# Kernel tuning notes

Measured on AMD Instinct MI355X. Metric: run time of the kernel, lower is better.

The kernel has to match this reference:

```python
import jax, jax.numpy as jnp
import numpy as np

B, N, D = 64, 128, 32
P = N * (N - 1)          # ordered pairs
H1, H2, HF = 32, 32, 16  # layer_widths=(32,32), final_widths=(16,)
EPS = 1e-5
SLOPE = 0.01             # LeakyReLU default


def _leaky(x):
    return jnp.where(x >= 0, x, SLOPE * x)


def setup_inputs() -> dict:
    key = jax.random.key(0)
    ks = jax.random.split(key, 16)
    # all ordered pairs (i, j), i != j, grouped by source i
    src = np.repeat(np.arange(N), N - 1)
    tgt = np.array([j for i in range(N) for j in range(N) if j != i])
    s = 0.1
    return {
        "inputs": jax.random.normal(ks[0], (B, N, D), jnp.float32),
        "src": jnp.asarray(src, jnp.int32),
        "tgt": jnp.asarray(tgt, jnp.int32),
        # edge MLP: Linear(2D,32) -> BN1d(P) -> LeakyReLU -> Linear(32,32) -> LeakyReLU -> Linear(32, 1+D)
        "W1": jax.random.normal(ks[1], (2 * D, H1), jnp.float32) * s,
        "b1": jnp.zeros((H1,), jnp.float32),
        "g1": jnp.ones((P,), jnp.float32),
        "be1": jnp.zeros((P,), jnp.float32),
        "W2": jax.random.normal(ks[2], (H1, H2), jnp.float32) * s,
        "b2": jnp.zeros((H2,), jnp.float32),
        "W3": jax.random.normal(ks[3], (H2, 1 + D), jnp.float32) * s,
        "b3": jnp.zeros((1 + D,), jnp.float32),
        # final MLP: Linear(2D,16) -> BN1d(16) -> LeakyReLU -> Linear(16, D)
        "Wf1": jax.random.normal(ks[4], (2 * D, HF), jnp.float32) * s,
        "bf1": jnp.zeros((HF,), jnp.float32),
        "gf": jnp.ones((HF,), jnp.float32),
        "bef": jnp.zeros((HF,), jnp.float32),
        "Wf2": jax.random.normal(ks[5], (HF, D), jnp.float32) * s,
        "bf2": jnp.zeros((D,), jnp.float32),
    }


def reference(inputs, src, tgt, W1, b1, g1, be1, W2, b2, W3, b3,
              Wf1, bf1, gf, bef, Wf2, bf2):
    b, n, d = inputs.shape
    # gather pair features: (B, P, 2D)
    paired = jnp.concatenate([inputs[:, src], inputs[:, tgt]], axis=2)
    h = paired @ W1 + b1                              # (B, P, H1)
    # BatchNorm1d(P) on (B, P, H1): normalize per pair channel over (batch, feat)
    m = h.mean(axis=(0, 2), keepdims=True)
    v = h.var(axis=(0, 2), keepdims=True)
    h = (h - m) * jax.lax.rsqrt(v + EPS) * g1[None, :, None] + be1[None, :, None]
    h = _leaky(h) @ W2 + b2
    h = _leaky(h) @ W3 + b3                           # (B, P, 1+D)
    edges = jax.nn.sigmoid(h[..., :1])                # (B, P, 1)
    messages = h[..., 1:]                             # (B, P, D)
    weighted = edges * messages
    # segment-sum over the (N-1) senders per source node
    agg = weighted.reshape(b, n, n - 1, d).sum(axis=2)  # (B, N, D)
    sm = jnp.concatenate([inputs, agg], axis=2).reshape(-1, 2 * d)
    f = sm @ Wf1 + bf1                                # (B*N, HF)
    mf = f.mean(axis=0)
    vf = f.var(axis=0)
    f = (f - mf) * jax.lax.rsqrt(vf + EPS) * gf + bef
    out = _leaky(f) @ Wf2 + bf2
    return edges[..., 0], out.reshape(b, n, d)
```

## Files before the change

### kernel.cpp

```cpp
#include <hip/hip_runtime.h>
#include <hip/hip_bf16.h>
#include <math.h>

#define BB 64
#define NN 128
#define DD 32
#define PP (NN * (NN - 1))
#define EPSF 1e-5f

typedef __attribute__((ext_vector_type(8))) short bf16x8;
typedef __attribute__((ext_vector_type(4))) float f32x4;

static __device__ __forceinline__ unsigned short f2bf(float x) {
    unsigned u = __builtin_bit_cast(unsigned, x);
    u += 0x7fff + ((u >> 16) & 1);
    return (unsigned short)(u >> 16);
}
static __device__ __forceinline__ unsigned pk2bf(float a, float b) {
    return (unsigned)f2bf(a) | ((unsigned)f2bf(b) << 16);
}
static __device__ __forceinline__ float leakyf(float x) {
    return fmaxf(x, 0.01f * x);
}

__global__ __launch_bounds__(256) void proj_kernel(
    const float* __restrict__ inputs, const float* __restrict__ W1,
    const float* __restrict__ b1,
    const float* __restrict__ W2, const float* __restrict__ W3,
    float* __restrict__ AT, float* __restrict__ BT,
    unsigned short* __restrict__ ATh, unsigned short* __restrict__ BTh,
    float* __restrict__ SA, float* __restrict__ QA,
    float* __restrict__ SB, float* __restrict__ QB,
    unsigned short* __restrict__ W2p, unsigned short* __restrict__ W3p,
    float* __restrict__ fpartA, float* __restrict__ fpartB)
{
    __shared__ float Xs[64][33];
    __shared__ float W1s[64][32];
    __shared__ float red[4][4];

    int n = blockIdx.x, tid = threadIdx.x;

    for (int idx = tid; idx < 2048; idx += 256) {
        int b = idx >> 5, d = idx & 31;
        Xs[b][d] = inputs[((size_t)b << 12) + ((size_t)n << 5) + d];
        W1s[idx >> 5][idx & 31] = W1[idx];
    }
    __syncthreads();

    int j = tid & 31, rb = tid >> 5;
    float b1j = b1[j];
    float sa = 0.f, qa = 0.f, sb = 0.f, qb = 0.f;
    #pragma unroll
    for (int i = 0; i < 8; ++i) {
        int b = rb * 8 + i;
        float a = b1j, c = 0.f;
        #pragma unroll
        for (int k = 0; k < 32; ++k) {
            a += Xs[b][k] * W1s[k][j];
            c += Xs[b][k] * W1s[32 + k][j];
        }
        size_t off = ((size_t)n * 64 + b) * 32 + j;
        AT[off] = a;  BT[off] = c;
        ATh[off] = f2bf(a);  BTh[off] = f2bf(c);
        sa += a; qa += a * a; sb += c; qb += c * c;
    }
    #pragma unroll
    for (int off = 32; off > 0; off >>= 1) {
        sa += __shfl_down(sa, off, 64);
        qa += __shfl_down(qa, off, 64);
        sb += __shfl_down(sb, off, 64);
        qb += __shfl_down(qb, off, 64);
    }
    int w = tid >> 6;
    if ((tid & 63) == 0) { red[w][0] = sa; red[w][1] = qa; red[w][2] = sb; red[w][3] = qb; }
    __syncthreads();
    if (tid == 0) {
        SA[n] = red[0][0] + red[1][0] + red[2][0] + red[3][0];
        QA[n] = red[0][1] + red[1][1] + red[2][1] + red[3][1];
        SB[n] = red[0][2] + red[1][2] + red[2][2] + red[3][2];
        QB[n] = red[0][3] + red[1][3] + red[2][3] + red[3][3];
    }

    if (blockIdx.x == 0 && tid < 64) {
        int l = tid, nn2 = l & 15, kc = l >> 4;
        #pragma unroll
        for (int ct = 0; ct < 2; ++ct)
            #pragma unroll
            for (int jj = 0; jj < 8; ++jj) {
                int k = kc * 8 + jj;
                W2p[(ct * 64 + l) * 8 + jj] = f2bf(W2[k * 32 + ct * 16 + nn2]);
            }
        #pragma unroll
        for (int ct = 0; ct < 3; ++ct)
            #pragma unroll
            for (int jj = 0; jj < 8; ++jj) {
                int k = kc * 8 + jj;
                int c = ct * 16 + nn2;
                W3p[(ct * 64 + l) * 8 + jj] = f2bf(c < 33 ? W3[k * 33 + c] : 0.f);
            }
    }
    if (blockIdx.x == 1) {
        for (int idx = tid; idx < 1024; idx += 256) {
            fpartA[idx] = 0.f;
            fpartB[idx] = 0.f;
        }
    }
}

__global__ __launch_bounds__(256) void stats2_kernel(
    const unsigned short* __restrict__ ATh, const unsigned short* __restrict__ BTh,
    const float* __restrict__ SA, const float* __restrict__ QA,
    const float* __restrict__ SB, const float* __restrict__ QB,
    const float* __restrict__ g1, const float* __restrict__ be1,
    float* __restrict__ statA, float* __restrict__ statB)
{
    __shared__ __align__(16) float part[4][64][4];
    int tid = threadIdx.x;
    int lane = tid & 63, w = tid >> 6;
    int s0 = (blockIdx.x >> 3) * 16, t0 = (blockIdx.x & 7) * 16;

    int m = lane & 15, kc = lane >> 4;
    const unsigned short* abase = ATh + (size_t)(s0 + m) * 2048 + kc * 8 + w * 512;
    const unsigned short* bbase = BTh + (size_t)(t0 + m) * 2048 + kc * 8 + w * 512;

    f32x4 acc = {0.f, 0.f, 0.f, 0.f};
    #pragma unroll
    for (int step = 0; step < 16; ++step) {
        bf16x8 av = *(const bf16x8*)(abase + step * 32);
        bf16x8 bv = *(const bf16x8*)(bbase + step * 32);
        acc = __builtin_amdgcn_mfma_f32_16x16x32_bf16(av, bv, acc, 0, 0, 0);
    }
    *(f32x4*)&part[w][lane][0] = acc;
    __syncthreads();

    if (w == 0) {
        #pragma unroll
        for (int ww = 1; ww < 4; ++ww) {
            f32x4 o = *(const f32x4*)&part[ww][lane][0];
            acc[0] += o[0]; acc[1] += o[1]; acc[2] += o[2]; acc[3] += o[3];
        }
        int col = lane & 15, quad = lane >> 4;
        int t = t0 + col;
        float sbt = SB[t], qbt = QB[t];
        #pragma unroll
        for (int r = 0; r < 4; ++r) {
            int s = s0 + quad * 4 + r;
            if (s != t) {
                int e = t - (t > s);
                int p = s * 127 + e;
                float S = SA[s] + sbt;
                float Q = QA[s] + qbt + 2.f * acc[r];
                float mean = S * (1.f / 2048.f);
                float var  = Q * (1.f / 2048.f) - mean * mean;
                float inv  = rsqrtf(var + EPSF);
                float sc   = inv * g1[p];
                statA[p] = sc;
                statB[p] = be1[p] - mean * sc;
            }
        }
    }
}

__global__ __launch_bounds__(256) void edges_kernel(
    const float* __restrict__ AT, const float* __restrict__ BT,
    const float* __restrict__ statA, const float* __restrict__ statB,
    const unsigned short* __restrict__ W2p, const unsigned short* __restrict__ W3p,
    const float* __restrict__ b2, const float* __restrict__ b3,
    const float* __restrict__ inputs, const float* __restrict__ Wf1,
    const float* __restrict__ bf1,
    float* __restrict__ edges_out, float* __restrict__ agg,
    float* __restrict__ f, float* __restrict__ fpartA, float* __restrict__ fpartB)
{
    __shared__ __align__(16) unsigned short Abuf[8][64][8];
    __shared__ __align__(16) unsigned short Hbuf[8][64][8];
    __shared__ __align__(16) float evb[128];
    __shared__ float aggbuf[32];

    int tid = threadIdx.x;
    int b = blockIdx.x >> 7;
    int s = blockIdx.x & 127;

    if (tid < 32) aggbuf[tid] = 0.f;

    int e2 = tid >> 1;
    int half = tid & 1;
    int k0 = half * 16;
    int m = e2 & 15, r = e2 >> 4;
    const float* arow = AT + ((size_t)s * 64 + b) * 32;

    float nh[16];
    if (e2 < 127) {
        int t = e2 + (e2 >= s);
        int p = s * 127 + e2;
        float sc = statA[p], sh = statB[p];
        const float4* brow = (const float4*)(BT + ((size_t)t * 64 + b) * 32 + k0);
        const float4* ar4  = (const float4*)(arow + k0);
        #pragma unroll
        for (int q = 0; q < 4; ++q) {
            float4 bv = brow[q];
            float4 av = ar4[q];
            nh[4*q+0] = leakyf((av.x + bv.x) * sc + sh);
            nh[4*q+1] = leakyf((av.y + bv.y) * sc + sh);
            nh[4*q+2] = leakyf((av.z + bv.z) * sc + sh);
            nh[4*q+3] = leakyf((av.w + bv.w) * sc + sh);
        }
    } else {
        #pragma unroll
        for (int q = 0; q < 16; ++q) nh[q] = 0.f;
    }
    union { bf16x8 v; unsigned u[4]; } U0, U1;
    #pragma unroll
    for (int q = 0; q < 4; ++q) {
        U0.u[q] = pk2bf(nh[2*q], nh[2*q+1]);
        U1.u[q] = pk2bf(nh[8+2*q], nh[8+2*q+1]);
    }
    int L0 = 2 * half * 16 + m;
    *(bf16x8*)&Abuf[r][L0][0]      = U0.v;
    *(bf16x8*)&Abuf[r][L0 + 16][0] = U1.v;

    int lane = tid & 63;
    int w = tid >> 6;
    int col = lane & 15, q4 = (lane >> 4) * 4;
    bf16x8 wb2[2], wb3[3];
    wb2[0] = *(const bf16x8*)(W2p + (0 * 64 + lane) * 8);
    wb2[1] = *(const bf16x8*)(W2p + (1 * 64 + lane) * 8);
    wb3[0] = *(const bf16x8*)(W3p + (0 * 64 + lane) * 8);
    wb3[1] = *(const bf16x8*)(W3p + (1 * 64 + lane) * 8);
    wb3[2] = *(const bf16x8*)(W3p + (2 * 64 + lane) * 8);
    float b2c0 = b2[col], b2c1 = b2[16 + col];
    float b3c[3];
    #pragma unroll
    for (int ct = 0; ct < 3; ++ct) {
        int c = ct * 16 + col;
        b3c[ct] = (c < 33) ? b3[c] : 0.f;
    }
    __syncthreads();

    #pragma unroll
    for (int rt = 0; rt < 2; ++rt) {
        int r2 = w * 2 + rt;
        bf16x8 a = *(const bf16x8*)&Abuf[r2][lane][0];
        f32x4 c0 = {0.f, 0.f, 0.f, 0.f}, c1 = {0.f, 0.f, 0.f, 0.f};
        c0 = __builtin_amdgcn_mfma_f32_16x16x32_bf16(a, wb2[0], c0, 0, 0, 0);
        c1 = __builtin_amdgcn_mfma_f32_16x16x32_bf16(a, wb2[1], c1, 0, 0, 0);
        #pragma unroll
        for (int reg = 0; reg < 4; ++reg) {
            float x = leakyf(c0[reg] + b2c0);
            int c = col;
            Hbuf[r2][(c >> 3) * 16 + q4 + reg][c & 7] = f2bf(x);
            float y = leakyf(c1[reg] + b2c1);
            int c2 = 16 + col;
            Hbuf[r2][(c2 >> 3) * 16 + q4 + reg][c2 & 7] = f2bf(y);
        }
    }
    __syncthreads();

    f32x4 o[2][3];
    #pragma unroll
    for (int rt = 0; rt < 2; ++rt) {
        int r2 = w * 2 + rt;
        bf16x8 a2 = *(const bf16x8*)&Hbuf[r2][lane][0];
        #pragma unroll
        for (int ct = 0; ct < 3; ++ct) {
            f32x4 cc = {0.f, 0.f, 0.f, 0.f};
            o[rt][ct] = __builtin_amdgcn_mfma_f32_16x16x32_bf16(a2, wb3[ct], cc, 0, 0, 0);
        }
    }

    if (col == 0) {
        #pragma unroll
        for (int rt = 0; rt < 2; ++rt) {
            int r2 = w * 2 + rt;
            int row0 = r2 * 16 + q4;
            float e0 = 1.f / (1.f + __expf(-(o[rt][0][0] + b3c[0])));
            float e1 = 1.f / (1.f + __expf(-(o[rt][0][1] + b3c[0])));
            float e2v = 1.f / (1.f + __expf(-(o[rt][0][2] + b3c[0])));
            float e3 = 1.f / (1.f + __expf(-(o[rt][0][3] + b3c[0])));
            float4 ev4;
            ev4.x = e0; ev4.y = e1; ev4.z = e2v;
            ev4.w = (row0 == 124) ? 0.f : e3;
            *(float4*)&evb[row0] = ev4;
            float* ep = edges_out + (size_t)b * PP + s * 127 + row0;
            ep[0] = e0; ep[1] = e1; ep[2] = e2v;
            if (row0 != 124) ep[3] = e3;
        }
    }
    __syncthreads();

    #pragma unroll
    for (int ct = 0; ct < 3; ++ct) {
        int c = ct * 16 + col;
        if (c >= 1 && c <= 32) {
            float part = 0.f;
            #pragma unroll
            for (int rt = 0; rt < 2; ++rt) {
                int row0 = (w * 2 + rt) * 16 + q4;
                float4 ev4 = *(const float4*)&evb[row0];
                float bb3 = b3c[ct];
                part += ev4.x * (o[rt][ct][0] + bb3);
                part += ev4.y * (o[rt][ct][1] + bb3);
                part += ev4.z * (o[rt][ct][2] + bb3);
                part += ev4.w * (o[rt][ct][3] + bb3);
            }
            atomicAdd(&aggbuf[c - 1], part);
        }
    }
    __syncthreads();

    size_t row = (size_t)b * 128 + s;
    if (tid < 32) agg[row * 32 + tid] = aggbuf[tid];

    if (tid < 16) {
        const float* xrow = inputs + row * 32;
        float acc = bf1[tid];
        #pragma unroll
        for (int k = 0; k < 32; ++k) acc += xrow[k] * Wf1[k * 16 + tid];
        #pragma unroll
        for (int k = 0; k < 32; ++k) acc += aggbuf[k] * Wf1[(32 + k) * 16 + tid];
        f[row * 16 + tid] = acc;
        int bucket = blockIdx.x & 63;
        atomicAdd(&fpartA[bucket * 16 + tid], acc);
        atomicAdd(&fpartB[bucket * 16 + tid], acc * acc);
    }
}

__global__ __launch_bounds__(256) void out_kernel(
    const float* __restrict__ f,
    const float* __restrict__ fpartA, const float* __restrict__ fpartB,
    const float* __restrict__ gf, const float* __restrict__ bef,
    const float* __restrict__ Wf2, const float* __restrict__ bf2,
    float* __restrict__ outp)
{
    __shared__ float Wf2s[16][32];
    __shared__ float sc[16], sh[16];
    __shared__ float fs[8][16];

    int tid = threadIdx.x;
    for (int idx = tid; idx < 512; idx += 256)
        Wf2s[idx >> 5][idx & 31] = Wf2[idx];
    if (tid < 16) {
        float S = 0.f, Q = 0.f;
        #pragma unroll
        for (int g = 0; g < 64; ++g) {
            S += fpartA[g * 16 + tid];
            Q += fpartB[g * 16 + tid];
        }
        float mean = S * (1.f / 8192.f);
        float var  = Q * (1.f / 8192.f) - mean * mean;
        float inv  = rsqrtf(var + EPSF);
        float s    = inv * gf[tid];
        sc[tid] = s;
        sh[tid] = bef[tid] - mean * s;
    }
    int row0 = blockIdx.x * 8;
    if (tid < 128) {
        int r = tid >> 4, j = tid & 15;
        fs[r][j] = f[(size_t)(row0 + r) * 16 + j];
    }
    __syncthreads();

    int rl = tid >> 5, d = tid & 31;
    float acc = bf2[d];
    #pragma unroll
    for (int j = 0; j < 16; ++j) {
        float v = fs[rl][j] * sc[j] + sh[j];
        v = fmaxf(v, 0.01f * v);
        acc += v * Wf2s[j][d];
    }
    outp[(size_t)(row0 + rl) * 32 + d] = acc;
}

extern "C" void kernel_launch(void* const* d_in, const int* in_sizes, int n_in,
                              void* d_out, int out_size, void* d_ws, size_t ws_size,
                              hipStream_t stream) {
    const float* inputs = (const float*)d_in[0];
    const float* W1   = (const float*)d_in[3];
    const float* b1   = (const float*)d_in[4];
    const float* g1   = (const float*)d_in[5];
    const float* be1  = (const float*)d_in[6];
    const float* W2   = (const float*)d_in[7];
    const float* b2   = (const float*)d_in[8];
    const float* W3   = (const float*)d_in[9];
    const float* b3   = (const float*)d_in[10];
    const float* Wf1  = (const float*)d_in[11];
    const float* bf1  = (const float*)d_in[12];
    const float* gf   = (const float*)d_in[13];
    const float* bef  = (const float*)d_in[14];
    const float* Wf2  = (const float*)d_in[15];
    const float* bf2  = (const float*)d_in[16];

    float* ws    = (float*)d_ws;
    float* AT    = ws;
    float* BT    = AT + 262144;
    float* SA    = BT + 262144;
    float* QA    = SA + 128;
    float* SB    = QA + 128;
    float* QB    = SB + 128;
    float* statA = QB + 128;
    float* statB = statA + PP;
    float* region = statB + PP;
    unsigned short* ATh = (unsigned short*)region;
    unsigned short* BTh = ATh + 262144;
    float* agg = region;
    float* f   = region + 262144;
    float* fpartA = region + 393216;
    float* fpartB = fpartA + 1024;
    unsigned short* W2p = (unsigned short*)(fpartB + 1024);
    unsigned short* W3p = W2p + 1024;

    float* edges_out = (float*)d_out;
    float* outp      = edges_out + (size_t)BB * PP;

    proj_kernel<<<128, 256, 0, stream>>>(inputs, W1, b1, W2, W3,
                                         AT, BT, ATh, BTh, SA, QA, SB, QB,
                                         W2p, W3p, fpartA, fpartB);
    stats2_kernel<<<64, 256, 0, stream>>>(ATh, BTh, SA, QA, SB, QB,
                                          g1, be1, statA, statB);
    edges_kernel<<<BB * NN, 256, 0, stream>>>(AT, BT, statA, statB, W2p, W3p,
                                              b2, b3, inputs, Wf1, bf1,
                                              edges_out, agg, f, fpartA, fpartB);
    out_kernel<<<8192 / 8, 256, 0, stream>>>(f, fpartA, fpartB, gf, bef, Wf2, bf2, outp);
}
```

Baseline: 148.6 us.

## Fuse four kernels into one cooperative persistent kernel with grid syncs

Merges the projection, pair-statistics, edge MLP and output kernels into one persistent cooperative kernel of 512 blocks, separated by grid-wide syncs, with a four-launch phased fallback. This removes the launch gaps between kernels. Each phase now loops over work units, and the projection phase is re-split into 1024 smaller units whose partial sums are reduced later in the stats phase. The cost is grid-sync overhead, fewer resident blocks than the old 8192-block edge launch, and an occupancy query on every call.

```diff
diff --git a/kernel.cpp b/kernel.cpp
--- a/kernel.cpp
+++ b/kernel.cpp
@@ -1,12 +1,16 @@
 #include <hip/hip_runtime.h>
+#include <hip/hip_cooperative_groups.h>
 #include <hip/hip_bf16.h>
 #include <math.h>
+
+namespace cg = cooperative_groups;
 
 #define BB 64
 #define NN 128
 #define DD 32
 #define PP (NN * (NN - 1))
 #define EPSF 1e-5f
+#define NBLK 512
 
 typedef __attribute__((ext_vector_type(8))) short bf16x8;
 typedef __attribute__((ext_vector_type(4))) float f32x4;
@@ -16,408 +20,418 @@
     u += 0x7fff + ((u >> 16) & 1);
     return (unsigned short)(u >> 16);
 }
-static __device__ __forceinline__ unsigned pk2bf(float a, float b) {
-    return (unsigned)f2bf(a) | ((unsigned)f2bf(b) << 16);
-}
 static __device__ __forceinline__ float leakyf(float x) {
     return fmaxf(x, 0.01f * x);
 }
 
-__global__ __launch_bounds__(256) void proj_kernel(
-    const float* __restrict__ inputs, const float* __restrict__ W1,
-    const float* __restrict__ b1,
-    const float* __restrict__ W2, const float* __restrict__ W3,
-    float* __restrict__ AT, float* __restrict__ BT,
-    unsigned short* __restrict__ ATh, unsigned short* __restrict__ BTh,
-    float* __restrict__ SA, float* __restrict__ QA,
-    float* __restrict__ SB, float* __restrict__ QB,
-    unsigned short* __restrict__ W2p, unsigned short* __restrict__ W3p,
-    float* __restrict__ fpartA, float* __restrict__ fpartB)
+struct Params {
+    const float *inputs, *W1, *b1, *g1, *be1, *W2, *b2, *W3, *b3;
+    const float *Wf1, *bf1, *gf, *bef, *Wf2, *bf2;
+    float *AT, *BT;
+    unsigned short *ATh, *BTh;
+    float *SQp;
+    float *statA, *statB, *agg, *f, *fpartA, *fpartB;
+    unsigned short *W2p, *W3p;
+    float *edges_out, *outp;
+};
+
+__global__ __launch_bounds__(256, 2) void fused_kernel(Params P, int phase)
 {
-    __shared__ float Xs[64][33];
-    __shared__ float W1s[64][32];
-    __shared__ float red[4][4];
-
-    int n = blockIdx.x, tid = threadIdx.x;
-
-    for (int idx = tid; idx < 2048; idx += 256) {
-        int b = idx >> 5, d = idx & 31;
-        Xs[b][d] = inputs[((size_t)b << 12) + ((size_t)n << 5) + d];
-        W1s[idx >> 5][idx & 31] = W1[idx];
-    }
-    __syncthreads();
-
-    int j = tid & 31, rb = tid >> 5;
-    float b1j = b1[j];
-    float sa = 0.f, qa = 0.f, sb = 0.f, qb = 0.f;
-    #pragma unroll
-    for (int i = 0; i < 8; ++i) {
-        int b = rb * 8 + i;
-        float a = b1j, c = 0.f;
-        #pragma unroll
-        for (int k = 0; k < 32; ++k) {
-            a += Xs[b][k] * W1s[k][j];
-            c += Xs[b][k] * W1s[32 + k][j];
-        }
-        size_t off = ((size_t)n * 64 + b) * 32 + j;
-        AT[off] = a;  BT[off] = c;
-        ATh[off] = f2bf(a);  BTh[off] = f2bf(c);
-        sa += a; qa += a * a; sb += c; qb += c * c;
-    }
-    #pragma unroll
-    for (int off = 32; off > 0; off >>= 1) {
-        sa += __shfl_down(sa, off, 64);
-        qa += __shfl_down(qa, off, 64);
-        sb += __shfl_down(sb, off, 64);
-        qb += __shfl_down(qb, off, 64);
-    }
-    int w = tid >> 6;
-    if ((tid & 63) == 0) { red[w][0] = sa; red[w][1] = qa; red[w][2] = sb; red[w][3] = qb; }
-    __syncthreads();
-    if (tid == 0) {
-        SA[n] = red[0][0] + red[1][0] + red[2][0] + red[3][0];
-        QA[n] = red[0][1] + red[1][1] + red[2][1] + red[3][1];
-        SB[n] = red[0][2] + red[1][2] + red[2][2] + red[3][2];
-        QB[n] = red[0][3] + red[1][3] + red[2][3] + red[3][3];
-    }
-
-    if (blockIdx.x == 0 && tid < 64) {
-        int l = tid, nn2 = l & 15, kc = l >> 4;
-        #pragma unroll
-        for (int ct = 0; ct < 2; ++ct)
-            #pragma unroll
-            for (int jj = 0; jj < 8; ++jj) {
-                int k = kc * 8 + jj;
-                W2p[(ct * 64 + l) * 8 + jj] = f2bf(W2[k * 32 + ct * 16 + nn2]);
-            }
-        #pragma unroll
-        for (int ct = 0; ct < 3; ++ct)
-            #pragma unroll
-            for (int jj = 0; jj < 8; ++jj) {
-                int k = kc * 8 + jj;
-                int c = ct * 16 + nn2;
-                W3p[(ct * 64 + l) * 8 + jj] = f2bf(c < 33 ? W3[k * 33 + c] : 0.f);
-            }
-    }
-    if (blockIdx.x == 1) {
-        for (int idx = tid; idx < 1024; idx += 256) {
-            fpartA[idx] = 0.f;
-            fpartB[idx] = 0.f;
-        }
-    }
-}
-
-__global__ __launch_bounds__(256) void stats2_kernel(
-    const unsigned short* __restrict__ ATh, const unsigned short* __restrict__ BTh,
-    const float* __restrict__ SA, const float* __restrict__ QA,
-    const float* __restrict__ SB, const float* __restrict__ QB,
-    const float* __restrict__ g1, const float* __restrict__ be1,
-    float* __restrict__ statA, float* __restrict__ statB)
-{
-    __shared__ __align__(16) float part[4][64][4];
+    cg::grid_group grid = cg::this_grid();
+    const bool all = (phase < 0);
+    __shared__ __align__(16) char smem[17472];
     int tid = threadIdx.x;
-    int lane = tid & 63, w = tid >> 6;
-    int s0 = (blockIdx.x >> 3) * 16, t0 = (blockIdx.x & 7) * 16;
-
-    int m = lane & 15, kc = lane >> 4;
-    const unsigned short* abase = ATh + (size_t)(s0 + m) * 2048 + kc * 8 + w * 512;
-    const unsigned short* bbase = BTh + (size_t)(t0 + m) * 2048 + kc * 8 + w * 512;
-
-    f32x4 acc = {0.f, 0.f, 0.f, 0.f};
-    #pragma unroll
-    for (int step = 0; step < 16; ++step) {
-        bf16x8 av = *(const bf16x8*)(abase + step * 32);
-        bf16x8 bv = *(const bf16x8*)(bbase + step * 32);
-        acc = __builtin_amdgcn_mfma_f32_16x16x32_bf16(av, bv, acc, 0, 0, 0);
-    }
-    *(f32x4*)&part[w][lane][0] = acc;
-    __syncthreads();
-
-    if (w == 0) {
-        #pragma unroll
-        for (int ww = 1; ww < 4; ++ww) {
-            f32x4 o = *(const f32x4*)&part[ww][lane][0];
-            acc[0] += o[0]; acc[1] += o[1]; acc[2] += o[2]; acc[3] += o[3];
-        }
-        int col = lane & 15, quad = lane >> 4;
-        int t = t0 + col;
-        float sbt = SB[t], qbt = QB[t];
-        #pragma unroll
-        for (int r = 0; r < 4; ++r) {
-            int s = s0 + quad * 4 + r;
-            if (s != t) {
-                int e = t - (t > s);
-                int p = s * 127 + e;
-                float S = SA[s] + sbt;
-                float Q = QA[s] + qbt + 2.f * acc[r];
-                float mean = S * (1.f / 2048.f);
-                float var  = Q * (1.f / 2048.f) - mean * mean;
-                float inv  = rsqrtf(var + EPSF);
-                float sc   = inv * g1[p];
-                statA[p] = sc;
-                statB[p] = be1[p] - mean * sc;
-            }
-        }
-    }
-}
-
-__global__ __launch_bounds__(256) void edges_kernel(
-    const float* __restrict__ AT, const float* __restrict__ BT,
-    const float* __restrict__ statA, const float* __restrict__ statB,
-    const unsigned short* __restrict__ W2p, const unsigned short* __restrict__ W3p,
-    const float* __restrict__ b2, const float* __restrict__ b3,
-    const float* __restrict__ inputs, const float* __restrict__ Wf1,
-    const float* __restrict__ bf1,
-    float* __restrict__ edges_out, float* __restrict__ agg,
-    float* __restrict__ f, float* __restrict__ fpartA, float* __restrict__ fpartB)
-{
-    __shared__ __align__(16) unsigned short Abuf[8][64][8];
-    __shared__ __align__(16) unsigned short Hbuf[8][64][8];
-    __shared__ __align__(16) float evb[128];
-    __shared__ float aggbuf[32];
-
-    int tid = threadIdx.x;
-    int b = blockIdx.x >> 7;
-    int s = blockIdx.x & 127;
-
-    if (tid < 32) aggbuf[tid] = 0.f;
-
-    int e2 = tid >> 1;
-    int half = tid & 1;
-    int k0 = half * 16;
-    int m = e2 & 15, r = e2 >> 4;
-    const float* arow = AT + ((size_t)s * 64 + b) * 32;
-
-    float nh[16];
-    if (e2 < 127) {
-        int t = e2 + (e2 >= s);
-        int p = s * 127 + e2;
-        float sc = statA[p], sh = statB[p];
-        const float4* brow = (const float4*)(BT + ((size_t)t * 64 + b) * 32 + k0);
-        const float4* ar4  = (const float4*)(arow + k0);
-        #pragma unroll
-        for (int q = 0; q < 4; ++q) {
-            float4 bv = brow[q];
-            float4 av = ar4[q];
-            nh[4*q+0] = leakyf((av.x + bv.x) * sc + sh);
-            nh[4*q+1] = leakyf((av.y + bv.y) * sc + sh);
-            nh[4*q+2] = leakyf((av.z + bv.z) * sc + sh);
-            nh[4*q+3] = leakyf((av.w + bv.w) * sc + sh);
-        }
-    } else {
-        #pragma unroll
-        for (int q = 0; q < 16; ++q) nh[q] = 0.f;
-    }
-    union { bf16x8 v; unsigned u[4]; } U0, U1;
-    #pragma unroll
-    for (int q = 0; q < 4; ++q) {
-        U0.u[q] = pk2bf(nh[2*q], nh[2*q+1]);
-        U1.u[q] = pk2bf(nh[8+2*q], nh[8+2*q+1]);
-    }
-    int L0 = 2 * half * 16 + m;
-    *(bf16x8*)&Abuf[r][L0][0]      = U0.v;
-    *(bf16x8*)&Abuf[r][L0 + 16][0] = U1.v;
-
+    int bx = blockIdx.x;
     int lane = tid & 63;
     int w = tid >> 6;
-    int col = lane & 15, q4 = (lane >> 4) * 4;
-    bf16x8 wb2[2], wb3[3];
-    wb2[0] = *(const bf16x8*)(W2p + (0 * 64 + lane) * 8);
-    wb2[1] = *(const bf16x8*)(W2p + (1 * 64 + lane) * 8);
-    wb3[0] = *(const bf16x8*)(W3p + (0 * 64 + lane) * 8);
-    wb3[1] = *(const bf16x8*)(W3p + (1 * 64 + lane) * 8);
-    wb3[2] = *(const bf16x8*)(W3p + (2 * 64 + lane) * 8);
-    float b2c0 = b2[col], b2c1 = b2[16 + col];
-    float b3c[3];
-    #pragma unroll
-    for (int ct = 0; ct < 3; ++ct) {
-        int c = ct * 16 + col;
-        b3c[ct] = (c < 33) ? b3[c] : 0.f;
+
+    if (all || phase == 0) {
+        float* Xs  = (float*)smem;
+        float* W1s = Xs + 264;
+        float* red = W1s + 2048;
+
+        for (int idx = tid; idx < 2048; idx += 256) W1s[idx] = P.W1[idx];
+
+        int j = tid & 31, rb = tid >> 5;
+        float b1j = P.b1[j];
+
+        for (int unit = bx; unit < 1024; unit += NBLK) {
+            int n = unit >> 3, o = unit & 7;
+            int b = o * 8 + rb;
+            __syncthreads();
+            Xs[rb * 33 + j] = P.inputs[((size_t)b << 12) + ((size_t)n << 5) + j];
+            __syncthreads();
+
+            float a = b1j, c = 0.f;
+            #pragma unroll
+            for (int k = 0; k < 32; ++k) {
+                float x = Xs[rb * 33 + k];
+                a += x * W1s[k * 32 + j];
+                c += x * W1s[(32 + k) * 32 + j];
+            }
+            size_t off = ((size_t)n * 64 + b) * 32 + j;
+            P.AT[off] = a;  P.BT[off] = c;
+            P.ATh[off] = f2bf(a);  P.BTh[off] = f2bf(c);
+
+            float sa = a, qa = a * a, sb = c, qb = c * c;
+            #pragma unroll
+            for (int d = 32; d > 0; d >>= 1) {
+                sa += __shfl_down(sa, d, 64);
+                qa += __shfl_down(qa, d, 64);
+                sb += __shfl_down(sb, d, 64);
+                qb += __shfl_down(qb, d, 64);
+            }
+            if (lane == 0) { red[w*4+0] = sa; red[w*4+1] = qa; red[w*4+2] = sb; red[w*4+3] = qb; }
+            __syncthreads();
+            if (tid == 0) {
+                float4 v;
+                v.x = red[0] + red[4] + red[8]  + red[12];
+                v.y = red[1] + red[5] + red[9]  + red[13];
+                v.z = red[2] + red[6] + red[10] + red[14];
+                v.w = red[3] + red[7] + red[11] + red[15];
+                ((float4*)P.SQp)[n * 8 + o] = v;
+            }
+        }
+
+        if (bx == 0 && tid < 64) {
+            int l = tid, nn2 = l & 15, kc = l >> 4;
+            #pragma unroll
+            for (int ct = 0; ct < 2; ++ct)
+                #pragma unroll
+                for (int jj = 0; jj < 8; ++jj) {
+                    int k = kc * 8 + jj;
+                    P.W2p[(ct * 64 + l) * 8 + jj] = f2bf(P.W2[k * 32 + ct * 16 + nn2]);
+                }
+            #pragma unroll
+            for (int ct = 0; ct < 3; ++ct)
+                #pragma unroll
+                for (int jj = 0; jj < 8; ++jj) {
+                    int k = kc * 8 + jj;
+                    int c2 = ct * 16 + nn2;
+                    P.W3p[(ct * 64 + l) * 8 + jj] = f2bf(c2 < 33 ? P.W3[k * 33 + c2] : 0.f);
+                }
+        }
+        if (bx == 1) {
+            for (int idx = tid; idx < 1024; idx += 256) {
+                P.fpartA[idx] = 0.f;
+                P.fpartB[idx] = 0.f;
+            }
+        }
     }
-    __syncthreads();
-
-    #pragma unroll
-    for (int rt = 0; rt < 2; ++rt) {
-        int r2 = w * 2 + rt;
-        bf16x8 a = *(const bf16x8*)&Abuf[r2][lane][0];
-        f32x4 c0 = {0.f, 0.f, 0.f, 0.f}, c1 = {0.f, 0.f, 0.f, 0.f};
-        c0 = __builtin_amdgcn_mfma_f32_16x16x32_bf16(a, wb2[0], c0, 0, 0, 0);
-        c1 = __builtin_amdgcn_mfma_f32_16x16x32_bf16(a, wb2[1], c1, 0, 0, 0);
-        #pragma unroll
-        for (int reg = 0; reg < 4; ++reg) {
-            float x = leakyf(c0[reg] + b2c0);
-            int c = col;
-            Hbuf[r2][(c >> 3) * 16 + q4 + reg][c & 7] = f2bf(x);
-            float y = leakyf(c1[reg] + b2c1);
-            int c2 = 16 + col;
-            Hbuf[r2][(c2 >> 3) * 16 + q4 + reg][c2 & 7] = f2bf(y);
+    if (all) grid.sync();
+
+    if (all || phase == 1) {
+        float* part = (float*)smem;
+        if (bx < 64) {
+            int s0 = (bx >> 3) * 16, t0 = (bx & 7) * 16;
+            int m = lane & 15, kc = lane >> 4;
+            const unsigned short* abase = P.ATh + (size_t)(s0 + m) * 2048 + kc * 8 + w * 512;
+            const unsigned short* bbase = P.BTh + (size_t)(t0 + m) * 2048 + kc * 8 + w * 512;
+
+            f32x4 acc = {0.f, 0.f, 0.f, 0.f};
+            #pragma unroll
+            for (int step = 0; step < 16; ++step) {
+                bf16x8 av = *(const bf16x8*)(abase + step * 32);
+                bf16x8 bv = *(const bf16x8*)(bbase + step * 32);
+                acc = __builtin_amdgcn_mfma_f32_16x16x32_bf16(av, bv, acc, 0, 0, 0);
+            }
+            *(f32x4*)&part[(w * 64 + lane) * 4] = acc;
+            __syncthreads();
+
+            if (w == 0) {
+                #pragma unroll
+                for (int ww = 1; ww < 4; ++ww) {
+                    f32x4 o2 = *(const f32x4*)&part[(ww * 64 + lane) * 4];
+                    acc[0] += o2[0]; acc[1] += o2[1]; acc[2] += o2[2]; acc[3] += o2[3];
+                }
+                int col = lane & 15, quad = lane >> 4;
+                int t = t0 + col;
+                float sbt = 0.f, qbt = 0.f;
+                #pragma unroll
+                for (int o2 = 0; o2 < 8; ++o2) {
+                    float4 v = ((const float4*)P.SQp)[t * 8 + o2];
+                    sbt += v.z; qbt += v.w;
+                }
+                #pragma unroll
+                for (int r = 0; r < 4; ++r) {
+                    int s = s0 + quad * 4 + r;
+                    if (s != t) {
+                        float sas = 0.f, qas = 0.f;
+                        #pragma unroll
+                        for (int o2 = 0; o2 < 8; ++o2) {
+                            float4 v = ((const float4*)P.SQp)[s * 8 + o2];
+                            sas += v.x; qas += v.y;
+                        }
+                        int e = t - (t > s);
+                        int p = s * 127 + e;
+                        float S = sas + sbt;
+                        float Q = qas + qbt + 2.f * acc[r];
+                        float mean = S * (1.f / 2048.f);
+                        float var  = Q * (1.f / 2048.f) - mean * mean;
+                        float inv  = rsqrtf(var + EPSF);
+                        float sc   = inv * P.g1[p];
+                        P.statA[p] = sc;
+                        P.statB[p] = P.be1[p] - mean * sc;
+                    }
+                }
+            }
         }
     }
-    __syncthreads();
-
-    f32x4 o[2][3];
-    #pragma unroll
-    for (int rt = 0; rt < 2; ++rt) {
-        int r2 = w * 2 + rt;
-        bf16x8 a2 = *(const bf16x8*)&Hbuf[r2][lane][0];
+    if (all) grid.sync();
+
+    if (all || phase == 2) {
+        unsigned short* Abuf = (unsigned short*)smem;
+        unsigned short* Hbuf = Abuf + 4096;
+        float* evb    = (float*)(smem + 16384);
+        float* aggbuf = evb + 128;
+
+        int s = bx & 127;
+
+        int e2 = tid >> 1;
+        int half = tid & 1;
+        int k0 = half * 16;
+        int m = e2 & 15, r = e2 >> 4;
+        int L0 = 2 * half * 16 + m;
+        bool valid = (e2 < 127);
+        int t = valid ? (e2 + (e2 >= s)) : 0;
+        int pe = s * 127 + (valid ? e2 : 126);
+        float sc = 0.f, sh = 0.f;
+        if (valid) { sc = P.statA[pe]; sh = P.statB[pe]; }
+
+        int col = lane & 15, q4 = (lane >> 4) * 4;
+        bf16x8 wb2[2], wb3[3];
+        wb2[0] = *(const bf16x8*)(P.W2p + (0 * 64 + lane) * 8);
+        wb2[1] = *(const bf16x8*)(P.W2p + (1 * 64 + lane) * 8);
+        wb3[0] = *(const bf16x8*)(P.W3p + (0 * 64 + lane) * 8);
+        wb3[1] = *(const bf16x8*)(P.W3p + (1 * 64 + lane) * 8);
+        wb3[2] = *(const bf16x8*)(P.W3p + (2 * 64 + lane) * 8);
+        float b2c0 = P.b2[col], b2c1 = P.b2[16 + col];
+        float b3c[3];
         #pragma unroll
         for (int ct = 0; ct < 3; ++ct) {
-            f32x4 cc = {0.f, 0.f, 0.f, 0.f};
-            o[rt][ct] = __builtin_amdgcn_mfma_f32_16x16x32_bf16(a2, wb3[ct], cc, 0, 0, 0);
+            int c = ct * 16 + col;
+            b3c[ct] = (c < 33) ? P.b3[c] : 0.f;
+        }
+
+        for (int u = 0; u < 2; ++u) {
+            int o = (bx >> 7) + u * 4;
+            for (int bi = 0; bi < 8; ++bi) {
+                int b = o * 8 + bi;
+                __syncthreads();
+                if (tid < 32) aggbuf[tid] = 0.f;
+
+                float nh[16];
+                if (valid) {
+                    const float4* brow = (const float4*)(P.BT + ((size_t)t * 64 + b) * 32 + k0);
+                    const float4* ar4  = (const float4*)(P.AT + ((size_t)s * 64 + b) * 32 + k0);
+                    #pragma unroll
+                    for (int q = 0; q < 4; ++q) {
+                        float4 bv = brow[q];
+                        float4 av = ar4[q];
+                        nh[4*q+0] = leakyf((av.x + bv.x) * sc + sh);
+                        nh[4*q+1] = leakyf((av.y + bv.y) * sc + sh);
+                        nh[4*q+2] = leakyf((av.z + bv.z) * sc + sh);
+                        nh[4*q+3] = leakyf((av.w + bv.w) * sc + sh);
+                    }
+                } else {
+                    #pragma unroll
+                    for (int q = 0; q < 16; ++q) nh[q] = 0.f;
+                }
+                bf16x8 v0, v1;
+                #pragma unroll
+                for (int jj = 0; jj < 8; ++jj) {
+                    v0[jj] = (short)f2bf(nh[jj]);
+                    v1[jj] = (short)f2bf(nh[8 + jj]);
+                }
+                *(bf16x8*)&Abuf[((size_t)r * 64 + L0) * 8]        = v0;
+                *(bf16x8*)&Abuf[((size_t)r * 64 + L0 + 16) * 8]   = v1;
+                __syncthreads();
+
+                #pragma unroll
+                for (int rt = 0; rt < 2; ++rt) {
+                    int r2 = w * 2 + rt;
+                    bf16x8 a = *(const bf16x8*)&Abuf[((size_t)r2 * 64 + lane) * 8];
+                    f32x4 c0 = {0.f, 0.f, 0.f, 0.f}, c1 = {0.f, 0.f, 0.f, 0.f};
+                    c0 = __builtin_amdgcn_mfma_f32_16x16x32_bf16(a, wb2[0], c0, 0, 0, 0);
+                    c1 = __builtin_amdgcn_mfma_f32_16x16x32_bf16(a, wb2[1], c1, 0, 0, 0);
+                    #pragma unroll
+                    for (int reg = 0; reg < 4; ++reg) {
+                        float x = leakyf(c0[reg] + b2c0);
+                        int c = col;
+                        Hbuf[((size_t)r2 * 64 + (c >> 3) * 16 + q4 + reg) * 8 + (c & 7)] = f2bf(x);
+                        float y = leakyf(c1[reg] + b2c1);
+                        int c2 = 16 + col;
+                        Hbuf[((size_t)r2 * 64 + (c2 >> 3) * 16 + q4 + reg) * 8 + (c2 & 7)] = f2bf(y);
+                    }
+                }
+                __syncthreads();
+
+                f32x4 oo[2][3];
+                #pragma unroll
+                for (int rt = 0; rt < 2; ++rt) {
+                    int r2 = w * 2 + rt;
+                    bf16x8 a2 = *(const bf16x8*)&Hbuf[((size_t)r2 * 64 + lane) * 8];
+                    #pragma unroll
+                    for (int ct = 0; ct < 3; ++ct) {
+                        f32x4 cc = {0.f, 0.f, 0.f, 0.f};
+                        oo[rt][ct] = __builtin_amdgcn_mfma_f32_16x16x32_bf16(a2, wb3[ct], cc, 0, 0, 0);
+                    }
+                }
+
+                if (col == 0) {
+                    #pragma unroll
+                    for (int rt = 0; rt < 2; ++rt) {
+                        int row0 = (w * 2 + rt) * 16 + q4;
+                        float e0 = 1.f / (1.f + __expf(-(oo[rt][0][0] + b3c[0])));
+                        float e1 = 1.f / (1.f + __expf(-(oo[rt][0][1] + b3c[0])));
+                        float e2v = 1.f / (1.f + __expf(-(oo[rt][0][2] + b3c[0])));
+                        float e3 = 1.f / (1.f + __expf(-(oo[rt][0][3] + b3c[0])));
+                        float4 ev4;
+                        ev4.x = e0; ev4.y = e1; ev4.z = e2v;
+                        ev4.w = (row0 == 124) ? 0.f : e3;
+                        *(float4*)&evb[row0] = ev4;
+                        float* ep = P.edges_out + (size_t)b * PP + s * 127 + row0;
+                        ep[0] = e0; ep[1] = e1; ep[2] = e2v;
+                        if (row0 != 124) ep[3] = e3;
+                    }
+                }
+                __syncthreads();
+
+                #pragma unroll
+                for (int ct = 0; ct < 3; ++ct) {
+                    int c = ct * 16 + col;
+                    if (c >= 1 && c <= 32) {
+                        float part = 0.f;
+                        #pragma unroll
+                        for (int rt = 0; rt < 2; ++rt) {
+                            int row0 = (w * 2 + rt) * 16 + q4;
+                            float4 ev4 = *(const float4*)&evb[row0];
+                            float bb3 = b3c[ct];
+                            part += ev4.x * (oo[rt][ct][0] + bb3);
+                            part += ev4.y * (oo[rt][ct][1] + bb3);
+                            part += ev4.z * (oo[rt][ct][2] + bb3);
+                            part += ev4.w * (oo[rt][ct][3] + bb3);
+                        }
+                        atomicAdd(&aggbuf[c - 1], part);
+                    }
+                }
+                __syncthreads();
+
+                size_t row = (size_t)b * 128 + s;
+                if (tid < 32) P.agg[row * 32 + tid] = aggbuf[tid];
+                if (tid < 16) {
+                    const float* xrow = P.inputs + row * 32;
+                    float acc = P.bf1[tid];
+                    #pragma unroll
+                    for (int k = 0; k < 32; ++k) acc += xrow[k] * P.Wf1[k * 16 + tid];
+                    #pragma unroll
+                    for (int k = 0; k < 32; ++k) acc += aggbuf[k] * P.Wf1[(32 + k) * 16 + tid];
+                    P.f[row * 16 + tid] = acc;
+                    int bucket = ((bx << 3) + bi) & 63;
+                    atomicAdd(&P.fpartA[bucket * 16 + tid], acc);
+                    atomicAdd(&P.fpartB[bucket * 16 + tid], acc * acc);
+                }
+            }
         }
     }
-
-    if (col == 0) {
-        #pragma unroll
-        for (int rt = 0; rt < 2; ++rt) {
-            int r2 = w * 2 + rt;
-            int row0 = r2 * 16 + q4;
-            float e0 = 1.f / (1.f + __expf(-(o[rt][0][0] + b3c[0])));
-            float e1 = 1.f / (1.f + __expf(-(o[rt][0][1] + b3c[0])));
-            float e2v = 1.f / (1.f + __expf(-(o[rt][0][2] + b3c[0])));
-            float e3 = 1.f / (1.f + __expf(-(o[rt][0][3] + b3c[0])));
-            float4 ev4;
-            ev4.x = e0; ev4.y = e1; ev4.z = e2v;
-            ev4.w = (row0 == 124) ? 0.f : e3;
-            *(float4*)&evb[row0] = ev4;
-            float* ep = edges_out + (size_t)b * PP + s * 127 + row0;
-            ep[0] = e0; ep[1] = e1; ep[2] = e2v;
-            if (row0 != 124) ep[3] = e3;
+    if (all) grid.sync();
+
+    if (all || phase == 3) {
+        float* Wf2s = (float*)smem;
+        float* sc   = Wf2s + 512;
+        float* sh   = sc + 16;
+        float* fs   = sh + 16;
+
+        for (int idx = tid; idx < 512; idx += 256) Wf2s[idx] = P.Wf2[idx];
+        if (tid < 16) {
+            float S = 0.f, Q = 0.f;
+            #pragma unroll
+            for (int g = 0; g < 64; ++g) {
+                S += P.fpartA[g * 16 + tid];
+                Q += P.fpartB[g * 16 + tid];
+            }
+            float mean = S * (1.f / 8192.f);
+            float var  = Q * (1.f / 8192.f) - mean * mean;
+            float inv  = rsqrtf(var + EPSF);
+            float s2   = inv * P.gf[tid];
+            sc[tid] = s2;
+            sh[tid] = P.bef[tid] - mean * s2;
+        }
+
+        for (int u = 0; u < 2; ++u) {
+            int unit = bx + u * NBLK;
+            int row0 = unit * 8;
+            __syncthreads();
+            if (tid < 128) {
+                int r = tid >> 4, j = tid & 15;
+                fs[r * 16 + j] = P.f[(size_t)(row0 + r) * 16 + j];
+            }
+            __syncthreads();
+
+            int rl = tid >> 5, d = tid & 31;
+            float acc = P.bf2[d];
+            #pragma unroll
+            for (int j = 0; j < 16; ++j) {
+                float v = fs[rl * 16 + j] * sc[j] + sh[j];
+                v = leakyf(v);
+                acc += v * Wf2s[j * 32 + d];
+            }
+            P.outp[(size_t)(row0 + rl) * 32 + d] = acc;
         }
     }
-    __syncthreads();
-
-    #pragma unroll
-    for (int ct = 0; ct < 3; ++ct) {
-        int c = ct * 16 + col;
-        if (c >= 1 && c <= 32) {
-            float part = 0.f;
-            #pragma unroll
-            for (int rt = 0; rt < 2; ++rt) {
-                int row0 = (w * 2 + rt) * 16 + q4;
-                float4 ev4 = *(const float4*)&evb[row0];
-                float bb3 = b3c[ct];
-                part += ev4.x * (o[rt][ct][0] + bb3);
-                part += ev4.y * (o[rt][ct][1] + bb3);
-                part += ev4.z * (o[rt][ct][2] + bb3);
-                part += ev4.w * (o[rt][ct][3] + bb3);
-            }
-            atomicAdd(&aggbuf[c - 1], part);
-        }
-    }
-    __syncthreads();
-
-    size_t row = (size_t)b * 128 + s;
-    if (tid < 32) agg[row * 32 + tid] = aggbuf[tid];
-
-    if (tid < 16) {
-        const float* xrow = inputs + row * 32;
-        float acc = bf1[tid];
-        #pragma unroll
-        for (int k = 0; k < 32; ++k) acc += xrow[k] * Wf1[k * 16 + tid];
-        #pragma unroll
-        for (int k = 0; k < 32; ++k) acc += aggbuf[k] * Wf1[(32 + k) * 16 + tid];
-        f[row * 16 + tid] = acc;
-        int bucket = blockIdx.x & 63;
-        atomicAdd(&fpartA[bucket * 16 + tid], acc);
-        atomicAdd(&fpartB[bucket * 16 + tid], acc * acc);
-    }
-}
-
-__global__ __launch_bounds__(256) void out_kernel(
-    const float* __restrict__ f,
-    const float* __restrict__ fpartA, const float* __restrict__ fpartB,
-    const float* __restrict__ gf, const float* __restrict__ bef,
-    const float* __restrict__ Wf2, const float* __restrict__ bf2,
-    float* __restrict__ outp)
-{
-    __shared__ float Wf2s[16][32];
-    __shared__ float sc[16], sh[16];
-    __shared__ float fs[8][16];
-
-    int tid = threadIdx.x;
-    for (int idx = tid; idx < 512; idx += 256)
-        Wf2s[idx >> 5][idx & 31] = Wf2[idx];
-    if (tid < 16) {
-        float S = 0.f, Q = 0.f;
-        #pragma unroll
-        for (int g = 0; g < 64; ++g) {
-            S += fpartA[g * 16 + tid];
-            Q += fpartB[g * 16 + tid];
-        }
-        float mean = S * (1.f / 8192.f);
-        float var  = Q * (1.f / 8192.f) - mean * mean;
-        float inv  = rsqrtf(var + EPSF);
-        float s    = inv * gf[tid];
-        sc[tid] = s;
-        sh[tid] = bef[tid] - mean * s;
-    }
-    int row0 = blockIdx.x * 8;
-    if (tid < 128) {
-        int r = tid >> 4, j = tid & 15;
-        fs[r][j] = f[(size_t)(row0 + r) * 16 + j];
-    }
-    __syncthreads();
-
-    int rl = tid >> 5, d = tid & 31;
-    float acc = bf2[d];
-    #pragma unroll
-    for (int j = 0; j < 16; ++j) {
-        float v = fs[rl][j] * sc[j] + sh[j];
-        v = fmaxf(v, 0.01f * v);
-        acc += v * Wf2s[j][d];
-    }
-    outp[(size_t)(row0 + rl) * 32 + d] = acc;
 }
 
 extern "C" void kernel_launch(void* const* d_in, const int* in_sizes, int n_in,
                               void* d_out, int out_size, void* d_ws, size_t ws_size,
                               hipStream_t stream) {
-    const float* inputs = (const float*)d_in[0];
-    const float* W1   = (const float*)d_in[3];
-    const float* b1   = (const float*)d_in[4];
-    const float* g1   = (const float*)d_in[5];
-    const float* be1  = (const float*)d_in[6];
-    const float* W2   = (const float*)d_in[7];
-    const float* b2   = (const float*)d_in[8];
-    const float* W3   = (const float*)d_in[9];
-    const float* b3   = (const float*)d_in[10];
-    const float* Wf1  = (const float*)d_in[11];
-    const float* bf1  = (const float*)d_in[12];
-    const float* gf   = (const float*)d_in[13];
-    const float* bef  = (const float*)d_in[14];
-    const float* Wf2  = (const float*)d_in[15];
-    const float* bf2  = (const float*)d_in[16];
-
-    float* ws    = (float*)d_ws;
-    float* AT    = ws;
-    float* BT    = AT + 262144;
-    float* SA    = BT + 262144;
-    float* QA    = SA + 128;
-    float* SB    = QA + 128;
-    float* QB    = SB + 128;
-    float* statA = QB + 128;
-    float* statB = statA + PP;
-    float* region = statB + PP;
-    unsigned short* ATh = (unsigned short*)region;
-    unsigned short* BTh = ATh + 262144;
-    float* agg = region;
-    float* f   = region + 262144;
-    float* fpartA = region + 393216;
-    float* fpartB = fpartA + 1024;
-    unsigned short* W2p = (unsigned short*)(fpartB + 1024);
-    unsigned short* W3p = W2p + 1024;
-
-    float* edges_out = (float*)d_out;
-    float* outp      = edges_out + (size_t)BB * PP;
-
-    proj_kernel<<<128, 256, 0, stream>>>(inputs, W1, b1, W2, W3,
-                                         AT, BT, ATh, BTh, SA, QA, SB, QB,
-                                         W2p, W3p, fpartA, fpartB);
-    stats2_kernel<<<64, 256, 0, stream>>>(ATh, BTh, SA, QA, SB, QB,
-                                          g1, be1, statA, statB);
-    edges_kernel<<<BB * NN, 256, 0, stream>>>(AT, BT, statA, statB, W2p, W3p,
-                                              b2, b3, inputs, Wf1, bf1,
-                                              edges_out, agg, f, fpartA, fpartB);
-    out_kernel<<<8192 / 8, 256, 0, stream>>>(f, fpartA, fpartB, gf, bef, Wf2, bf2, outp);
+    Params P;
+    P.inputs = (const float*)d_in[0];
+    P.W1  = (const float*)d_in[3];
+    P.b1  = (const float*)d_in[4];
+    P.g1  = (const float*)d_in[5];
+    P.be1 = (const float*)d_in[6];
+    P.W2  = (const float*)d_in[7];
+    P.b2  = (const float*)d_in[8];
+    P.W3  = (const float*)d_in[9];
+    P.b3  = (const float*)d_in[10];
+    P.Wf1 = (const float*)d_in[11];
+    P.bf1 = (const float*)d_in[12];
+    P.gf  = (const float*)d_in[13];
+    P.bef = (const float*)d_in[14];
+    P.Wf2 = (const float*)d_in[15];
+    P.bf2 = (const float*)d_in[16];
+
+    float* ws = (float*)d_ws;
+    P.AT     = ws;
+    P.BT     = ws + 262144;
+    P.ATh    = (unsigned short*)(ws + 524288);
+    P.BTh    = P.ATh + 262144;
+    P.SQp    = ws + 786432;
+    P.statA  = ws + 790528;
+    P.statB  = ws + 806784;
+    P.agg    = ws + 823040;
+    P.f      = ws + 1085184;
+    P.fpartA = ws + 1216256;
+    P.fpartB = ws + 1217280;
+    P.W2p    = (unsigned short*)(ws + 1218304);
+    P.W3p    = P.W2p + 1024;
+
+    P.edges_out = (float*)d_out;
+    P.outp      = P.edges_out + (size_t)BB * PP;
+
+    int maxBlocksPerCU = 0;
+    hipError_t qerr = hipOccupancyMaxActiveBlocksPerMultiprocessor(
+        &maxBlocksPerCU, (const void*)fused_kernel, 256, 0);
+    bool coop_ok = (qerr == hipSuccess) && (maxBlocksPerCU >= 2);
+
+    if (coop_ok) {
+        int phase = -1;
+        void* args[] = { &P, &phase };
+        hipError_t lerr = hipLaunchCooperativeKernel(
+            (void*)fused_kernel, dim3(NBLK), dim3(256), args, 0, stream);
+        if (lerr == hipSuccess) return;
+        (void)hipGetLastError();
+    }
+    for (int ph = 0; ph < 4; ++ph)
+        fused_kernel<<<NBLK, 256, 0, stream>>>(P, ph);
 }
```

Result: slower. 409.9 us (+175.9%).
